# Optimization experiments

Measured on AMD Instinct MI355X. Metric: run time of the kernel, lower is better.

## Reference

```python
import jax, jax.numpy as jnp
import numpy as np

B, S, H, DH = 2, 2048, 24, 32
E = H * DH  # 768


def setup_inputs() -> dict:
    key = jax.random.key(0)
    ks = jax.random.split(key, 7)
    embedding = jax.random.normal(ks[0], (B, S, E), dtype=jnp.float32)
    mask = jax.random.randint(ks[1], (B, S, S), 0, 2).astype(bool)
    # per-head QKV weights (applied as x @ W, equivalent param to torch Linear W.T)
    Wq = jax.random.normal(ks[2], (H, DH, DH), dtype=jnp.float32) * 0.05
    Wk = jax.random.normal(ks[3], (H, DH, DH), dtype=jnp.float32) * 0.05
    Wv = jax.random.normal(ks[4], (H, DH, DH), dtype=jnp.float32) * 0.05
    Wo = jax.random.normal(ks[5], (E, E), dtype=jnp.float32) * 0.02
    bo = jax.random.normal(ks[6], (E,), dtype=jnp.float32) * 0.02
    return {"embedding": embedding, "mask": mask, "Wq": Wq, "Wk": Wk,
            "Wv": Wv, "Wo": Wo, "bo": bo}


def reference(embedding, mask, Wq, Wk, Wv, Wo, bo):
    # split channels into heads: [B,S,H,DH]
    xh = embedding.reshape(B, S, H, DH)
    # per-head projections (batched over heads)
    Q = jnp.einsum('bshd,hde->bhse', xh, Wq)
    K = jnp.einsum('bshd,hde->bhse', xh, Wk)
    V = jnp.einsum('bshd,hde->bhse', xh, Wv)
    scale = 1.0 / jnp.sqrt(jnp.float32(DH))
    scores = jnp.einsum('bhqd,bhkd->bhqk', Q, K) * scale
    # faithful quirk: masked positions set to -1e-6 (not -inf)
    scores = jnp.where(mask[:, None, :, :], scores, jnp.float32(-1e-6))
    probs = jax.nn.softmax(scores, axis=-1)
    out = jnp.einsum('bhqk,bhkd->bqhd', probs, V)  # [B,S,H,DH]
    out = out.reshape(B, S, E)  # concat heads along feature dim
    return out @ Wo.T + bo
```

## Files before the change

kernel.cpp:

```cpp
#include <hip/hip_runtime.h>
#include <hip/hip_bf16.h>

#define B_  2
#define S_  2048
#define H_  24
#define DH_ 32
#define E_  768
#define SW_ (S_/32)

#define NB_QKV  ((S_/64)*(B_*H_))
#define NB_MASK ((B_*S_*S_)/256)
#define NB_WO   ((E_*E_)/1024)

typedef __attribute__((ext_vector_type(8))) short short8;
typedef __attribute__((ext_vector_type(4))) float f32x4;
typedef _Float16 half8  __attribute__((ext_vector_type(8)));
typedef _Float16 half2v __attribute__((ext_vector_type(2)));
typedef __fp16   fp16x2 __attribute__((ext_vector_type(2)));

static __device__ __forceinline__ half2v cvt2h(float a, float b) {
    fp16x2 t = __builtin_amdgcn_cvt_pkrtz(a, b);
    return __builtin_bit_cast(half2v, t);
}

static __device__ __forceinline__ short4 pack4(float a, float b, float c, float d) {
    union { __hip_bfloat162 h[2]; short4 s; } u;
    u.h[0] = __float22bfloat162_rn(make_float2(a, b));
    u.h[1] = __float22bfloat162_rn(make_float2(c, d));
    return u.s;
}
static __device__ __forceinline__ short8 pack8f(const float* a, const float* b) {
    union { __hip_bfloat162 h[4]; short8 s; } u;
    u.h[0] = __float22bfloat162_rn(make_float2(a[0], a[1]));
    u.h[1] = __float22bfloat162_rn(make_float2(a[2], a[3]));
    u.h[2] = __float22bfloat162_rn(make_float2(b[0], b[1]));
    u.h[3] = __float22bfloat162_rn(make_float2(b[2], b[3]));
    return u.s;
}
static __device__ __forceinline__ short8 pack8(float4 a, float4 b) {
    union { __hip_bfloat162 h[4]; short8 s; } u;
    u.h[0] = __float22bfloat162_rn(make_float2(a.x, a.y));
    u.h[1] = __float22bfloat162_rn(make_float2(a.z, a.w));
    u.h[2] = __float22bfloat162_rn(make_float2(b.x, b.y));
    u.h[3] = __float22bfloat162_rn(make_float2(b.z, b.w));
    return u.s;
}
static __device__ __forceinline__ short8 wfrag(const float* __restrict__ Wb,
                                               int quad, int eo) {
    float w[8];
#pragma unroll
    for (int j = 0; j < 8; ++j) w[j] = Wb[(quad * 8 + j) * 32 + eo];
    return pack8f(w, w + 4);
}

#define QSCALE  0.25503487f

static __device__ __forceinline__ float mexp2(float s, unsigned mw, int pos) {
    const int m = __builtin_amdgcn_sbfe((int)mw, pos, 1);
    const int xi = __builtin_bit_cast(int, s) & m;
    return __builtin_amdgcn_exp2f(__builtin_bit_cast(float, xi));
}

__global__ __launch_bounds__(256) void prep_qkv_kernel(
    const float* __restrict__ x, const int* __restrict__ mask,
    const float* __restrict__ Wo,
    const float* __restrict__ Wq, const float* __restrict__ Wk,
    const float* __restrict__ Wv,
    __hip_bfloat16* __restrict__ Qo,
    __hip_bfloat16* __restrict__ Ko,
    _Float16* __restrict__ Vto,
    unsigned int* __restrict__ mbits, _Float16* __restrict__ Wob)
{
    const int bx = blockIdx.x;
    if (bx < NB_QKV) {
        const int bh   = bx >> 5;
        const int b    = bh / H_;
        const int h    = bh - b * H_;
        const int wave = threadIdx.x >> 6;
        const int lane = threadIdx.x & 63;
        const int col  = lane & 15;
        const int quad = lane >> 4;
        const int sw   = (bx & 31) * 64 + wave * 16;
        const int s    = sw + col;

        const float* xp = x + ((size_t)b * S_ + s) * E_ + h * DH_ + quad * 8;
        const float4 xa = *reinterpret_cast<const float4*>(xp);
        const float4 xb = *reinterpret_cast<const float4*>(xp + 4);
        const short8 xf = pack8(xa, xb);

        const int wb = h * DH_ * DH_;
        const short8 aQ0 = wfrag(Wq + wb, quad, col);
        const short8 aQ1 = wfrag(Wq + wb, quad, col + 16);
        const short8 aK0 = wfrag(Wk + wb, quad, col);
        const short8 aK1 = wfrag(Wk + wb, quad, col + 16);
        const short8 bV0 = wfrag(Wv + wb, quad, col);
        const short8 bV1 = wfrag(Wv + wb, quad, col + 16);

        const f32x4 z = {0.f, 0.f, 0.f, 0.f};
        const f32x4 qt0 = __builtin_amdgcn_mfma_f32_16x16x32_bf16(aQ0, xf, z, 0, 0, 0);
        const f32x4 qt1 = __builtin_amdgcn_mfma_f32_16x16x32_bf16(aQ1, xf, z, 0, 0, 0);
        const f32x4 kt0 = __builtin_amdgcn_mfma_f32_16x16x32_bf16(aK0, xf, z, 0, 0, 0);
        const f32x4 kt1 = __builtin_amdgcn_mfma_f32_16x16x32_bf16(aK1, xf, z, 0, 0, 0);
        const f32x4 vv0 = __builtin_amdgcn_mfma_f32_16x16x32_bf16(xf, bV0, z, 0, 0, 0);
        const f32x4 vv1 = __builtin_amdgcn_mfma_f32_16x16x32_bf16(xf, bV1, z, 0, 0, 0);

        __hip_bfloat16* qrow = Qo + ((size_t)bh * S_ + s) * DH_;
        *reinterpret_cast<short4*>(qrow + quad * 4) =
            pack4(qt0[0] * QSCALE, qt0[1] * QSCALE, qt0[2] * QSCALE, qt0[3] * QSCALE);
        *reinterpret_cast<short4*>(qrow + 16 + quad * 4) =
            pack4(qt1[0] * QSCALE, qt1[1] * QSCALE, qt1[2] * QSCALE, qt1[3] * QSCALE);

        const int t32  = s & 31;
        const int slot = (s & ~31) | (((t32 >> 2) & 1) << 4)
                       | (((t32 >> 3) << 2) | (t32 & 3));
        __hip_bfloat16* krow = Ko + ((size_t)bh * S_ + slot) * DH_;
        *reinterpret_cast<short4*>(krow + quad * 4)      = pack4(kt0[0], kt0[1], kt0[2], kt0[3]);
        *reinterpret_cast<short4*>(krow + 16 + quad * 4) = pack4(kt1[0], kt1[1], kt1[2], kt1[3]);

        const int sb = sw + quad * 4;
        union { half2v h[2]; uint2 u; } v0u, v1u;
        v0u.h[0] = cvt2h(vv0[0], vv0[1]); v0u.h[1] = cvt2h(vv0[2], vv0[3]);
        v1u.h[0] = cvt2h(vv1[0], vv1[1]); v1u.h[1] = cvt2h(vv1[2], vv1[3]);
        *reinterpret_cast<uint2*>(Vto + ((size_t)bh * DH_ + col) * S_ + sb)      = v0u.u;
        *reinterpret_cast<uint2*>(Vto + ((size_t)bh * DH_ + 16 + col) * S_ + sb) = v1u.u;
    } else if (bx < NB_QKV + NB_MASK) {
        const int idx  = (bx - NB_QKV) * 256 + threadIdx.x;
        const int lane = threadIdx.x & 63;
        const unsigned long long bal = __ballot(mask[idx] != 0);
        if (lane == 0) {
            uint2 w;
            w.x = (unsigned int)(bal & 0xffffffffull);
            w.y = (unsigned int)(bal >> 32);
            *reinterpret_cast<uint2*>(mbits + (idx >> 5)) = w;
        }
    } else {
        const int i = ((bx - NB_QKV - NB_MASK) * 256 + threadIdx.x) * 4;
        const float4 w = *reinterpret_cast<const float4*>(Wo + i);
        union { half2v h[2]; uint2 u; } uu;
        uu.h[0] = cvt2h(w.x, w.y);
        uu.h[1] = cvt2h(w.z, w.w);
        *reinterpret_cast<uint2*>(Wob + i) = uu.u;
    }
}

__global__ __launch_bounds__(64) void attn_kernel(
    const __hip_bfloat16* __restrict__ Q,
    const __hip_bfloat16* __restrict__ K,
    const _Float16* __restrict__ Vt,
    const unsigned int* __restrict__ mbits,
    _Float16* __restrict__ Opart,
    float* __restrict__ lpart,
    int parts)
{
    const int bid  = blockIdx.x;
    const int xcd  = bid & 7;
    const int t_   = bid >> 3;
    const int bh   = xcd * 6 + (t_ % 6);
    const int rest = t_ / 6;
    const int qsub = rest & 31;
    const int part = rest >> 5;

    const int b    = bh / H_;
    const int h    = bh - b * H_;
    const int niter = S_ / (64 * parts);
    const int kbeg  = part * (S_ / parts);
    const int lane = threadIdx.x & 63;
    const int col  = lane & 15;
    const int quad = lane >> 4;
    const int q0   = qsub * 64;

    const __hip_bfloat16* Qbh = Q  + (size_t)bh * S_ * DH_;
    const __hip_bfloat16* Kbh = K  + (size_t)bh * S_ * DH_;
    const _Float16*       Vbh = Vt + (size_t)bh * DH_ * S_;

    short8 qf[4];
#pragma unroll
    for (int t = 0; t < 4; ++t)
        qf[t] = *reinterpret_cast<const short8*>(
            Qbh + (size_t)(q0 + t * 16 + col) * DH_ + quad * 8);

    const __hip_bfloat16* Kp  = Kbh + (size_t)(kbeg + col) * DH_ + quad * 8;
    const _Float16*       Vp0 = Vbh + (size_t)col * S_ + kbeg + quad * 8;
    const _Float16*       Vp1 = Vbh + (size_t)(16 + col) * S_ + kbeg + quad * 8;
    const unsigned int* mbb = mbits + (size_t)b * S_ * SW_ + (kbeg >> 5);
    const unsigned int* mp[4];
#pragma unroll
    for (int t = 0; t < 4; ++t)
        mp[t] = mbb + (size_t)(q0 + t * 16 + col) * SW_;

    const int posL = quad * 8;
    const int posH = quad * 8 + 4;

    union { uint4 u; half8 v; } onesu;
    onesu.u = make_uint4(0x3C003C00u, 0x3C003C00u, 0x3C003C00u, 0x3C003C00u);
    const half8 ones_h = onesu.v;

    f32x4 o0a[4], o1a[4], la[4];
#pragma unroll
    for (int t = 0; t < 4; ++t) {
        o0a[t] = (f32x4){0.f,0.f,0.f,0.f};
        o1a[t] = (f32x4){0.f,0.f,0.f,0.f};
        la[t]  = (f32x4){0.f,0.f,0.f,0.f};
    }

    for (int it = 0; it < niter; ++it) {
        uint2 mw[4];
#pragma unroll
        for (int t = 0; t < 4; ++t)
            mw[t] = *reinterpret_cast<const uint2*>(mp[t]);

        const short8 kA0 = *reinterpret_cast<const short8*>(Kp);
        const short8 kA1 = *reinterpret_cast<const short8*>(Kp + 16 * DH_);
        const half8  vA0 = *reinterpret_cast<const half8*>(Vp0);
        const half8  vA1 = *reinterpret_cast<const half8*>(Vp1);
        const short8 kB0 = *reinterpret_cast<const short8*>(Kp + 32 * DH_);
        const short8 kB1 = *reinterpret_cast<const short8*>(Kp + 48 * DH_);
        const half8  vB0 = *reinterpret_cast<const half8*>(Vp0 + 32);
        const half8  vB1 = *reinterpret_cast<const half8*>(Vp1 + 32);

        const f32x4 z = {0.f, 0.f, 0.f, 0.f};

        f32x4 s0[4], s1[4];
#pragma unroll
        for (int t = 0; t < 4; ++t) {
            s0[t] = __builtin_amdgcn_mfma_f32_16x16x32_bf16(kA0, qf[t], z, 0, 0, 0);
            s1[t] = __builtin_amdgcn_mfma_f32_16x16x32_bf16(kA1, qf[t], z, 0, 0, 0);
        }
#pragma unroll
        for (int t = 0; t < 4; ++t) {
            float p0[4], p1[4];
#pragma unroll
            for (int r = 0; r < 4; ++r) {
                p0[r] = mexp2(s0[t][r], mw[t].x, posL + r);
                p1[r] = mexp2(s1[t][r], mw[t].x, posH + r);
            }
            union { half2v h[4]; half8 v; } pu;
            pu.h[0] = cvt2h(p0[0], p0[1]);
            pu.h[1] = cvt2h(p0[2], p0[3]);
            pu.h[2] = cvt2h(p1[0], p1[1]);
            pu.h[3] = cvt2h(p1[2], p1[3]);
            const half8 pf = pu.v;
            o0a[t] = __builtin_amdgcn_mfma_f32_16x16x32_f16(vA0, pf, o0a[t], 0, 0, 0);
            o1a[t] = __builtin_amdgcn_mfma_f32_16x16x32_f16(vA1, pf, o1a[t], 0, 0, 0);
            la[t]  = __builtin_amdgcn_mfma_f32_16x16x32_f16(ones_h, pf, la[t], 0, 0, 0);
        }

#pragma unroll
        for (int t = 0; t < 4; ++t) {
            s0[t] = __builtin_amdgcn_mfma_f32_16x16x32_bf16(kB0, qf[t], z, 0, 0, 0);
            s1[t] = __builtin_amdgcn_mfma_f32_16x16x32_bf16(kB1, qf[t], z, 0, 0, 0);
        }
#pragma unroll
        for (int t = 0; t < 4; ++t) {
            float p0[4], p1[4];
#pragma unroll
            for (int r = 0; r < 4; ++r) {
                p0[r] = mexp2(s0[t][r], mw[t].y, posL + r);
                p1[r] = mexp2(s1[t][r], mw[t].y, posH + r);
            }
            union { half2v h[4]; half8 v; } pu;
            pu.h[0] = cvt2h(p0[0], p0[1]);
            pu.h[1] = cvt2h(p0[2], p0[3]);
            pu.h[2] = cvt2h(p1[0], p1[1]);
            pu.h[3] = cvt2h(p1[2], p1[3]);
            const half8 pf = pu.v;
            o0a[t] = __builtin_amdgcn_mfma_f32_16x16x32_f16(vB0, pf, o0a[t], 0, 0, 0);
            o1a[t] = __builtin_amdgcn_mfma_f32_16x16x32_f16(vB1, pf, o1a[t], 0, 0, 0);
            la[t]  = __builtin_amdgcn_mfma_f32_16x16x32_f16(ones_h, pf, la[t], 0, 0, 0);
        }

        Kp  += 64 * DH_;
        Vp0 += 64;
        Vp1 += 64;
#pragma unroll
        for (int t = 0; t < 4; ++t) mp[t] += 2;
    }

    _Float16* Ob = Opart + (size_t)part * B_ * S_ * E_;
    float* lp = lpart + (size_t)part * B_ * H_ * S_ + (size_t)bh * S_;
#pragma unroll
    for (int t = 0; t < 4; ++t) {
        union { half2v h[2]; uint2 u; } u0, u1;
        u0.h[0] = cvt2h(o0a[t][0], o0a[t][1]);
        u0.h[1] = cvt2h(o0a[t][2], o0a[t][3]);
        u1.h[0] = cvt2h(o1a[t][0], o1a[t][1]);
        u1.h[1] = cvt2h(o1a[t][2], o1a[t][3]);
        _Float16* orow = Ob + ((size_t)b * S_ + q0 + t * 16 + col) * E_ + h * DH_;
        *reinterpret_cast<uint2*>(orow + quad * 4)      = u0.u;
        *reinterpret_cast<uint2*>(orow + 16 + quad * 4) = u1.u;
        if (quad == 0) lp[q0 + t * 16 + col] = la[t][0];
    }
}

template <int PARTS>
__global__ __launch_bounds__(256) void proj_kernel(
    const _Float16* __restrict__ Opart,
    const float* __restrict__ lpart,
    const _Float16* __restrict__ Wob,
    const float* __restrict__ bo,
    float* __restrict__ out)
{
    const int wave = threadIdx.x >> 6;
    const int lane = threadIdx.x & 63;
    const int col  = lane & 15;
    const int quad = lane >> 4;
    const int m0   = blockIdx.x * 16;
    const int n0   = blockIdx.y * 256 + wave * 64;

    const int m = m0 + col;
    const int b = m / S_;
    const int s = m - b * S_;
    const float* lpb = lpart + (size_t)(b * H_) * S_ + s;

    f32x4 acc[4] = {{0.f,0.f,0.f,0.f},{0.f,0.f,0.f,0.f},
                    {0.f,0.f,0.f,0.f},{0.f,0.f,0.f,0.f}};
    for (int k0 = 0; k0 < E_; k0 += 32) {
        const int h = k0 >> 5;
        const size_t aofs = (size_t)m * E_ + k0 + quad * 8;

        float l = 0.f;
#pragma unroll
        for (int pp = 0; pp < PARTS; ++pp)
            l += lpb[(size_t)pp * B_ * H_ * S_ + (size_t)h * S_];
        const float linv = __builtin_amdgcn_rcpf(l);
        const half2v lv = cvt2h(linv, linv);

        union UA { uint4 u; half2v h[4]; half8 v; } ua;
        ua.u = *reinterpret_cast<const uint4*>(Opart + aofs);
#pragma unroll
        for (int pp = 1; pp < PARTS; ++pp) {
            union UA ub;
            ub.u = *reinterpret_cast<const uint4*>(
                Opart + (size_t)pp * B_ * S_ * E_ + aofs);
#pragma unroll
            for (int i = 0; i < 4; ++i) ua.h[i] += ub.h[i];
        }
#pragma unroll
        for (int i = 0; i < 4; ++i) ua.h[i] *= lv;
        const half8 af = ua.v;

#pragma unroll
        for (int j = 0; j < 4; ++j) {
            union UA wb;
            wb.u = *reinterpret_cast<const uint4*>(
                Wob + (size_t)(n0 + j * 16 + col) * E_ + k0 + quad * 8);
            acc[j] = __builtin_amdgcn_mfma_f32_16x16x32_f16(af, wb.v, acc[j], 0, 0, 0);
        }
    }
#pragma unroll
    for (int j = 0; j < 4; ++j) {
        const int n = n0 + j * 16 + col;
        const float bias = bo[n];
#pragma unroll
        for (int r = 0; r < 4; ++r) {
            const int mm = m0 + quad * 4 + r;
            out[(size_t)mm * E_ + n] = acc[j][r] + bias;
        }
    }
}

extern "C" void kernel_launch(void* const* d_in, const int* in_sizes, int n_in,
                              void* d_out, int out_size, void* d_ws, size_t ws_size,
                              hipStream_t stream)
{
    const float* emb = (const float*)d_in[0];
    const int*   msk = (const int*)d_in[1];
    const float* Wq  = (const float*)d_in[2];
    const float* Wk  = (const float*)d_in[3];
    const float* Wv  = (const float*)d_in[4];
    const float* Wo  = (const float*)d_in[5];
    const float* bo  = (const float*)d_in[6];
    float* out = (float*)d_out;

    const size_t nqkv = (size_t)B_ * H_ * S_ * DH_;
    char* p = (char*)d_ws;
    __hip_bfloat16* Q    = (__hip_bfloat16*)p;  p += nqkv * 2;
    __hip_bfloat16* Kp   = (__hip_bfloat16*)p;  p += nqkv * 2;
    _Float16*      Vt    = (_Float16*)p;        p += nqkv * 2;
    unsigned int*  mbits = (unsigned int*)p;    p += (size_t)B_ * S_ * SW_ * 4;
    _Float16*      Wob   = (_Float16*)p;        p += (size_t)E_ * E_ * 2;
    _Float16*      Op    = (_Float16*)p;
    const size_t base = (size_t)(p - (char*)d_ws);

    int parts = 1;
    {
        const size_t need = base + (size_t)2 * nqkv * 2
                          + (size_t)2 * B_ * H_ * S_ * 4;
        if (ws_size >= need) parts = 2;
    }
    float* lpart = (float*)(Op + (size_t)parts * nqkv);

    prep_qkv_kernel<<<NB_QKV + NB_MASK + NB_WO, 256, 0, stream>>>(
        emb, msk, Wo, Wq, Wk, Wv, Q, Kp, Vt, mbits, Wob);
    attn_kernel<<<1536 * parts, 64, 0, stream>>>(
        Q, Kp, Vt, mbits, Op, lpart, parts);
    if (parts == 2)
        proj_kernel<2><<<dim3((B_ * S_) / 16, E_ / 256), 256, 0, stream>>>(
            Op, lpart, Wob, bo, out);
    else
        proj_kernel<1><<<dim3((B_ * S_) / 16, E_ / 256), 256, 0, stream>>>(
            Op, lpart, Wob, bo, out);
}
```

Before: 233.1 us.

## Double-buffer K and mask register loads across attention loop iterations

The attention main loop is unrolled by two, and the K fragments and mask words for the next 64-key block are prefetched into a second register set while the current block is computed. The goal is to hide global-load latency behind the MFMA and exp work, since this kernel runs only one 64-thread wave per block. The launch bounds also gain a minimum-blocks hint of 3, which may push the compiler to cap register use. Risks: higher register pressure or spills, the loop now assumes an even iteration count, and the final prefetch reads one block past the key range, which can touch memory past the end of the buffer.

```diff
diff --git a/kernel.cpp b/kernel.cpp
--- a/kernel.cpp
+++ b/kernel.cpp
@@ -143,7 +143,7 @@
     }
 }
 
-__global__ __launch_bounds__(64) void attn_kernel(
+__global__ __launch_bounds__(64, 3) void attn_kernel(
     const __hip_bfloat16* __restrict__ Q,
     const __hip_bfloat16* __restrict__ K,
     const _Float16* __restrict__ Vt,
@@ -179,14 +179,15 @@
         qf[t] = *reinterpret_cast<const short8*>(
             Qbh + (size_t)(q0 + t * 16 + col) * DH_ + quad * 8);
 
-    const __hip_bfloat16* Kp  = Kbh + (size_t)(kbeg + col) * DH_ + quad * 8;
-    const _Float16*       Vp0 = Vbh + (size_t)col * S_ + kbeg + quad * 8;
-    const _Float16*       Vp1 = Vbh + (size_t)(16 + col) * S_ + kbeg + quad * 8;
+    const _Float16* Vp0 = Vbh + (size_t)col * S_ + kbeg + quad * 8;
+    const _Float16* Vp1 = Vbh + (size_t)(16 + col) * S_ + kbeg + quad * 8;
+
+    const __hip_bfloat16* Kf = Kbh + (size_t)(kbeg + col) * DH_ + quad * 8;
     const unsigned int* mbb = mbits + (size_t)b * S_ * SW_ + (kbeg >> 5);
-    const unsigned int* mp[4];
-#pragma unroll
-    for (int t = 0; t < 4; ++t)
-        mp[t] = mbb + (size_t)(q0 + t * 16 + col) * SW_;
+    const unsigned int* mf0 = mbb + (size_t)(q0 +  0 + col) * SW_;
+    const unsigned int* mf1 = mbb + (size_t)(q0 + 16 + col) * SW_;
+    const unsigned int* mf2 = mbb + (size_t)(q0 + 32 + col) * SW_;
+    const unsigned int* mf3 = mbb + (size_t)(q0 + 48 + col) * SW_;
 
     const int posL = quad * 8;
     const int posH = quad * 8 + 4;
@@ -203,21 +204,40 @@
         la[t]  = (f32x4){0.f,0.f,0.f,0.f};
     }
 
-    for (int it = 0; it < niter; ++it) {
-        uint2 mw[4];
-#pragma unroll
-        for (int t = 0; t < 4; ++t)
-            mw[t] = *reinterpret_cast<const uint2*>(mp[t]);
-
-        const short8 kA0 = *reinterpret_cast<const short8*>(Kp);
-        const short8 kA1 = *reinterpret_cast<const short8*>(Kp + 16 * DH_);
-        const half8  vA0 = *reinterpret_cast<const half8*>(Vp0);
-        const half8  vA1 = *reinterpret_cast<const half8*>(Vp1);
-        const short8 kB0 = *reinterpret_cast<const short8*>(Kp + 32 * DH_);
-        const short8 kB1 = *reinterpret_cast<const short8*>(Kp + 48 * DH_);
-        const half8  vB0 = *reinterpret_cast<const half8*>(Vp0 + 32);
-        const half8  vB1 = *reinterpret_cast<const half8*>(Vp1 + 32);
-
+    short8 ak0, ak1, ak2, ak3; uint2 am0, am1, am2, am3;
+    short8 bk0, bk1, bk2, bk3; uint2 bm0, bm1, bm2, bm3;
+
+    auto load_a = [&]() {
+        ak0 = *reinterpret_cast<const short8*>(Kf);
+        ak1 = *reinterpret_cast<const short8*>(Kf + 16 * DH_);
+        ak2 = *reinterpret_cast<const short8*>(Kf + 32 * DH_);
+        ak3 = *reinterpret_cast<const short8*>(Kf + 48 * DH_);
+        am0 = *reinterpret_cast<const uint2*>(mf0);
+        am1 = *reinterpret_cast<const uint2*>(mf1);
+        am2 = *reinterpret_cast<const uint2*>(mf2);
+        am3 = *reinterpret_cast<const uint2*>(mf3);
+        Kf += 64 * DH_; mf0 += 2; mf1 += 2; mf2 += 2; mf3 += 2;
+    };
+    auto load_b = [&]() {
+        bk0 = *reinterpret_cast<const short8*>(Kf);
+        bk1 = *reinterpret_cast<const short8*>(Kf + 16 * DH_);
+        bk2 = *reinterpret_cast<const short8*>(Kf + 32 * DH_);
+        bk3 = *reinterpret_cast<const short8*>(Kf + 48 * DH_);
+        bm0 = *reinterpret_cast<const uint2*>(mf0);
+        bm1 = *reinterpret_cast<const uint2*>(mf1);
+        bm2 = *reinterpret_cast<const uint2*>(mf2);
+        bm3 = *reinterpret_cast<const uint2*>(mf3);
+        Kf += 64 * DH_; mf0 += 2; mf1 += 2; mf2 += 2; mf3 += 2;
+    };
+
+    auto compute = [&](const short8& kA0, const short8& kA1,
+                       const short8& kB0, const short8& kB1,
+                       uint2 w0, uint2 w1, uint2 w2, uint2 w3) {
+        const half8 vA0 = *reinterpret_cast<const half8*>(Vp0);
+        const half8 vA1 = *reinterpret_cast<const half8*>(Vp1);
+        const half8 vB0 = *reinterpret_cast<const half8*>(Vp0 + 32);
+        const half8 vB1 = *reinterpret_cast<const half8*>(Vp1 + 32);
+        const uint2 mw[4] = {w0, w1, w2, w3};
         const f32x4 z = {0.f, 0.f, 0.f, 0.f};
 
         f32x4 s0[4], s1[4];
@@ -269,11 +289,16 @@
             la[t]  = __builtin_amdgcn_mfma_f32_16x16x32_f16(ones_h, pf, la[t], 0, 0, 0);
         }
 
-        Kp  += 64 * DH_;
         Vp0 += 64;
         Vp1 += 64;
-#pragma unroll
-        for (int t = 0; t < 4; ++t) mp[t] += 2;
+    };
+
+    load_a();
+    for (int it = 0; it < niter; it += 2) {
+        load_b();
+        compute(ak0, ak1, ak2, ak3, am0, am1, am2, am3);
+        load_a();
+        compute(bk0, bk1, bk2, bk3, bm0, bm1, bm2, bm3);
     }
 
     _Float16* Ob = Opart + (size_t)part * B_ * S_ * E_;
```

Result: faster. 217.4 us (-6.7%).
